# Kernel tuning notes

Hardware: AMD Instinct MI355X
Metric: run time of the kernel (lower is better)

Reference implementation:

```python
import jax, jax.numpy as jnp
import numpy as np

B, S, D, H = 2, 2048, 1024, 16
HD = D // H

def setup_inputs() -> dict:
    key = jax.random.key(0)
    ks = jax.random.split(key, 9)
    s = 1.0 / np.sqrt(D)
    return {
        "x": jax.random.normal(ks[0], (B, S, D), jnp.float32),
        "Wq": jax.random.normal(ks[1], (D, D), jnp.float32) * s,
        "bq": jnp.zeros((D,), jnp.float32),
        "Wk": jax.random.normal(ks[2], (D, D), jnp.float32) * s,
        "bk": jnp.zeros((D,), jnp.float32),
        "Wv": jax.random.normal(ks[3], (D, D), jnp.float32) * s,
        "bv": jnp.zeros((D,), jnp.float32),
        "Wo": jax.random.normal(ks[4], (D, D), jnp.float32) * s,
        "bo": jnp.zeros((D,), jnp.float32),
    }

def reference(x, Wq, bq, Wk, bk, Wv, bv, Wo, bo):
    b, s, d = x.shape
    def split_heads(t):
        return t.reshape(b, s, H, HD).transpose(0, 2, 1, 3)  # [B,H,S,HD]
    q = split_heads(x @ Wq + bq)
    k = split_heads(x @ Wk + bk)
    v = split_heads(x @ Wv + bv)
    scores = jnp.einsum('bhqd,bhkd->bhqk', q, k) / jnp.sqrt(jnp.float32(HD))
    causal = jnp.tril(jnp.ones((s, s), bool))  # True = keep
    scores = jnp.where(causal, scores, -jnp.inf)
    attn = jax.nn.softmax(scores, axis=-1)
    out = jnp.einsum('bhqk,bhkd->bhqd', attn, v)  # [B,H,S,HD]
    out = out.transpose(0, 2, 1, 3).reshape(b, s, d)
    return out @ Wo + bo
```

## Files before the change

kernel.cpp:

```cpp
#include <hip/hip_runtime.h>

typedef unsigned short u16;
typedef unsigned int u32;
typedef __attribute__((ext_vector_type(8))) short bf16x8;
typedef __attribute__((ext_vector_type(4))) float f32x4;
typedef __attribute__((ext_vector_type(16))) float f32x16;

#define BB 2
#define SS 2048
#define DD 1024
#define HH 16
#define HD 64
#define MM (BB * SS)

__device__ inline float u2f(u32 u) { return __uint_as_float(u); }
__device__ inline u16 f2bf(float f) {
  u32 u = __float_as_uint(f);
  return (u16)((u + 0x7fffu + ((u >> 16) & 1u)) >> 16);
}

typedef const __attribute__((address_space(1))) void* gas_ptr;
typedef __attribute__((address_space(3))) void* las_ptr;
__device__ __forceinline__ void gll16(const void* g, void* l) {
  __builtin_amdgcn_global_load_lds((gas_ptr)g, (las_ptr)l, 16, 0, 0);
}

__device__ __forceinline__ u32 pk2(float a, float b) {
  return (__float_as_uint(a) >> 16) | (__float_as_uint(b) & 0xffff0000u);
}

__global__ __launch_bounds__(256) void prep(const float* __restrict__ x, u16* __restrict__ xb,
                                            const float* __restrict__ W0, const float* __restrict__ W1,
                                            const float* __restrict__ W2, const float* __restrict__ W3,
                                            u16* __restrict__ Wt) {
  int z = blockIdx.z;
  int t = threadIdx.x;
  if (z >= 4) {
    int gid = (z - 4) * 256 + blockIdx.y * 16 + blockIdx.x;
    int i = (gid * 256 + t) * 8;
    float4 a = *(const float4*)(x + i);
    float4 b = *(const float4*)(x + i + 4);
    uint4 o;
    o.x = (u32)f2bf(a.x) | ((u32)f2bf(a.y) << 16);
    o.y = (u32)f2bf(a.z) | ((u32)f2bf(a.w) << 16);
    o.z = (u32)f2bf(b.x) | ((u32)f2bf(b.y) << 16);
    o.w = (u32)f2bf(b.z) | ((u32)f2bf(b.w) << 16);
    *(uint4*)(xb + i) = o;
    return;
  }
  const float* W = (z == 0) ? W0 : (z == 1) ? W1 : (z == 2) ? W2 : W3;
  u16* out = Wt + (size_t)z * (DD * DD);
  __shared__ __align__(16) u16 T[64][72];
  int n0 = blockIdx.x * 64, k0 = blockIdx.y * 64;
#pragma unroll
  for (int p = 0; p < 4; ++p) {
    int kr = (t >> 4) + p * 16;
    int c4 = (t & 15) * 4;
    float4 v = *(const float4*)&W[(size_t)(k0 + kr) * DD + n0 + c4];
    T[c4 + 0][kr] = f2bf(v.x);
    T[c4 + 1][kr] = f2bf(v.y);
    T[c4 + 2][kr] = f2bf(v.z);
    T[c4 + 3][kr] = f2bf(v.w);
  }
  __syncthreads();
#pragma unroll
  for (int p = 0; p < 2; ++p) {
    int n = (t >> 3) + p * 32;
    int c8 = (t & 7) * 8;
    uint4 v = *(const uint4*)&T[n][c8];
    *(uint4*)&out[(size_t)(n0 + n) * DD + k0 + c8] = v;
  }
}

__global__ __launch_bounds__(256, 3) void gemm_qkv(const u16* __restrict__ xb, const u16* __restrict__ Wt,
                                                   const float* __restrict__ bq, const float* __restrict__ bk,
                                                   const float* __restrict__ bv,
                                                   u16* __restrict__ Qb, u16* __restrict__ Kb, u16* __restrict__ Vtb) {
  __shared__ __align__(16) u16 As[2][128 * 32];
  __shared__ __align__(16) u16 Bs[2][128 * 32];
  const int tid = threadIdx.x, lane = tid & 63, wv = tid >> 6;
  const int wm = (wv >> 1) * 64, wn = (wv & 1) * 64;
  const int l16 = lane & 15, quad = lane >> 4;

  const int id = blockIdx.x;
  const int xcd = id & 7, inner = id >> 3;
  const int mg = xcd >> 1, ng = xcd & 1;
  const int im = inner & 7, rest = inner >> 3;
  const int in_ = rest & 3, z = rest >> 2;
  const int m0 = (mg * 8 + im) * 128, n0 = (ng * 4 + in_) * 128;

  const u16* Bt = Wt + (size_t)z * (DD * DD);
  const float* bias = (z == 0) ? bq : (z == 1) ? bk : bv;

  const int r0 = tid >> 2, k8 = (tid & 3) << 3;
  const u16* Ap0 = &xb[(size_t)(m0 + r0) * DD + k8];
  const u16* Ap1 = Ap0 + (size_t)64 * DD;
  const u16* Bp0 = &Bt[(size_t)(n0 + r0) * DD + k8];
  const u16* Bp1 = Bp0 + (size_t)64 * DD;

  gll16(Ap0, &As[0][wv * 512]);
  gll16(Ap1, &As[0][2048 + wv * 512]);
  gll16(Bp0, &Bs[0][wv * 512]);
  gll16(Bp1, &Bs[0][2048 + wv * 512]);

  f32x4 acc[4][4];
  f32x4 zero = {0.f, 0.f, 0.f, 0.f};
#pragma unroll
  for (int i = 0; i < 4; ++i)
#pragma unroll
    for (int j = 0; j < 4; ++j) acc[i][j] = zero;

  __syncthreads();

  for (int kk = 0; kk < 32; ++kk) {
    const int cur = kk & 1;
    if (kk + 1 < 32) {
      const int nxt = cur ^ 1;
      const int ko = (kk + 1) * 32;
      gll16(Ap0 + ko, &As[nxt][wv * 512]);
      gll16(Ap1 + ko, &As[nxt][2048 + wv * 512]);
      gll16(Bp0 + ko, &Bs[nxt][wv * 512]);
      gll16(Bp1 + ko, &Bs[nxt][2048 + wv * 512]);
    }
    bf16x8 af[4], bg[4];
#pragma unroll
    for (int i = 0; i < 4; ++i) {
      af[i] = *(const bf16x8*)&As[cur][(wm + i * 16 + l16) * 32 + quad * 8];
      bg[i] = *(const bf16x8*)&Bs[cur][(wn + i * 16 + l16) * 32 + quad * 8];
    }
#pragma unroll
    for (int i = 0; i < 4; ++i)
#pragma unroll
      for (int j = 0; j < 4; ++j)
        acc[i][j] = __builtin_amdgcn_mfma_f32_16x16x32_bf16(af[i], bg[j], acc[i][j], 0, 0, 0);
    __syncthreads();
  }

  const float qsc = (z == 0) ? 0.180336880f : 1.0f;
  if (z == 2) {
#pragma unroll
    for (int i = 0; i < 4; ++i) {
#pragma unroll
      for (int j = 0; j < 4; ++j) {
        int col = n0 + wn + j * 16 + l16;
        float bcol = bias[col];
        int hh = col >> 6, dd = col & 63;
        int row0 = m0 + wm + i * 16;
        int bb = row0 >> 11, s0 = row0 & (SS - 1);
        int sbase = (s0 & ~63) + i * 16 + ((quad & 1) << 3) + ((quad >> 1) << 2);
        size_t base = (((size_t)((bb * HH + hh) * HD + dd)) << 11) + sbase;
        uint2 pv;
        pv.x = (u32)f2bf(acc[i][j][0] + bcol) | ((u32)f2bf(acc[i][j][1] + bcol) << 16);
        pv.y = (u32)f2bf(acc[i][j][2] + bcol) | ((u32)f2bf(acc[i][j][3] + bcol) << 16);
        *(uint2*)&Vtb[base] = pv;
      }
    }
  } else {
    u16* out = (z == 0) ? Qb : Kb;
#pragma unroll
    for (int i = 0; i < 4; ++i) {
#pragma unroll
      for (int j = 0; j < 4; ++j) {
        int col = n0 + wn + j * 16 + l16;
        float bcol = bias[col];
        int hh = col >> 6, dd = col & 63;
#pragma unroll
        for (int r = 0; r < 4; ++r) {
          int row = m0 + wm + i * 16 + quad * 4 + r;
          int bb = row >> 11, s = row & (SS - 1);
          out[((size_t)((bb * HH + hh) * SS + s) << 6) | dd] = f2bf((acc[i][j][r] + bcol) * qsc);
        }
      }
    }
  }
}

__global__ __launch_bounds__(256, 3) void gemm_out(const u16* __restrict__ Ub, const u16* __restrict__ Wot,
                                                   const float* __restrict__ bo, float* __restrict__ out) {
  __shared__ __align__(16) u16 As[2][128 * 32];
  __shared__ __align__(16) u16 Bs[2][64 * 32];
  const int tid = threadIdx.x, lane = tid & 63, wv = tid >> 6;
  const int wm = (wv >> 1) * 64, wn = (wv & 1) * 32;
  const int l16 = lane & 15, quad = lane >> 4;
  const int r0 = tid >> 2, k8 = (tid & 3) << 3;

  const int id = blockIdx.x;
  const int xcd = id & 7, inner = id >> 3;
  const int mg = xcd >> 1, ng = xcd & 1;
  const int im = inner & 7, in_ = inner >> 3;
  const int m0 = (mg * 8 + im) * 128, n0 = (ng * 8 + in_) * 64;

  const u16* Ap0 = &Ub[(size_t)(m0 + r0) * DD + k8];
  const u16* Ap1 = Ap0 + (size_t)64 * DD;
  const u16* Bp0 = &Wot[(size_t)(n0 + r0) * DD + k8];

  gll16(Ap0, &As[0][wv * 512]);
  gll16(Ap1, &As[0][2048 + wv * 512]);
  gll16(Bp0, &Bs[0][wv * 512]);

  f32x4 acc[4][2];
  f32x4 zero = {0.f, 0.f, 0.f, 0.f};
#pragma unroll
  for (int i = 0; i < 4; ++i) { acc[i][0] = zero; acc[i][1] = zero; }

  __syncthreads();

  for (int kk = 0; kk < 32; ++kk) {
    const int cur = kk & 1;
    if (kk + 1 < 32) {
      const int nxt = cur ^ 1;
      const int ko = (kk + 1) * 32;
      gll16(Ap0 + ko, &As[nxt][wv * 512]);
      gll16(Ap1 + ko, &As[nxt][2048 + wv * 512]);
      gll16(Bp0 + ko, &Bs[nxt][wv * 512]);
    }
    bf16x8 af[4], bg[2];
#pragma unroll
    for (int i = 0; i < 4; ++i) af[i] = *(const bf16x8*)&As[cur][(wm + i * 16 + l16) * 32 + quad * 8];
#pragma unroll
    for (int j = 0; j < 2; ++j) bg[j] = *(const bf16x8*)&Bs[cur][(wn + j * 16 + l16) * 32 + quad * 8];
#pragma unroll
    for (int i = 0; i < 4; ++i)
#pragma unroll
      for (int j = 0; j < 2; ++j)
        acc[i][j] = __builtin_amdgcn_mfma_f32_16x16x32_bf16(af[i], bg[j], acc[i][j], 0, 0, 0);
    __syncthreads();
  }

#pragma unroll
  for (int i = 0; i < 4; ++i) {
#pragma unroll
    for (int j = 0; j < 2; ++j) {
      int col = n0 + wn + j * 16 + l16;
      float bcol = bo[col];
#pragma unroll
      for (int r = 0; r < 4; ++r) {
        int row = m0 + wm + i * 16 + quad * 4 + r;
        out[(size_t)row * DD + col] = acc[i][j][r] + bcol;
      }
    }
  }
}

__global__ __launch_bounds__(256, 2) void attention_mfma(const u16* __restrict__ Q, const u16* __restrict__ K,
                                                         const u16* __restrict__ Vt, u16* __restrict__ Uo) {
  const int tid = threadIdx.x, lane = tid & 63, wv = tid >> 6;
  const int l31 = lane & 31, hi = lane >> 5;
  const int bh = blockIdx.x & 31;
  const int b = bh >> 4, h = bh & 15;
  const int g = blockIdx.x >> 5;
  const int qb = (blockIdx.x < 256) ? (15 - g) : (g - 8);
  const int q0 = qb * 128;
  const int qbase = q0 + wv * 32;
  const u16* Qh = Q + (size_t)(b * HH + h) * SS * HD;
  const u16* Kh = K + (size_t)(b * HH + h) * SS * HD;
  const u16* Vh = Vt + (size_t)(b * HH + h) * HD * SS;

  __shared__ __align__(16) u16 K_lds[2][4160];
  __shared__ __align__(16) u16 V_lds[2][4160];
  __shared__ float lsc[128];

  bf16x8 qf[4];
  {
    const u16* qp = &Qh[(size_t)(qbase + l31) * HD + 8 * hi];
#pragma unroll
    for (int m = 0; m < 4; ++m) qf[m] = *(const bf16x8*)(qp + 16 * m);
  }

  f32x16 o0, o1;
#pragma unroll
  for (int i = 0; i < 16; ++i) { o0[i] = 0.f; o1[i] = 0.f; }
  float lsum = 0.f;

  const int sr = tid >> 2, ci = tid & 3;
  const u16* Kg = &Kh[(size_t)sr * HD + ci * 8];
  const u16* Vg = &Vh[(size_t)sr * SS + ci * 8];
  const int ktiles = 2 * qb + 2;
  const int w0 = ci * 520 + sr * 8, w1 = (ci + 4) * 520 + sr * 8;

  uint4 ka = *(const uint4*)Kg, kb = *(const uint4*)(Kg + 32);
  uint4 va = *(const uint4*)Vg, vb = *(const uint4*)(Vg + 32);
  *(uint4*)&K_lds[0][w0] = ka;
  *(uint4*)&K_lds[0][w1] = kb;
  *(uint4*)&V_lds[0][w0] = va;
  *(uint4*)&V_lds[0][w1] = vb;
  {
    const u16* Kn = Kg + (size_t)64 * HD;
    const u16* Vn = Vg + 64;
    ka = *(const uint4*)Kn; kb = *(const uint4*)(Kn + 32);
    va = *(const uint4*)Vn; vb = *(const uint4*)(Vn + 32);
  }
  __syncthreads();

  for (int t = 0; t < ktiles; ++t) {
    const int cur = t & 1;
    if (64 * t <= qbase + 31) {
      f32x16 s0, s1;
#pragma unroll
      for (int i = 0; i < 16; ++i) { s0[i] = 0.f; s1[i] = 0.f; }
#pragma unroll
      for (int m = 0; m < 4; ++m) {
        const u16* kp = &K_lds[cur][(2 * m + hi) * 520 + l31 * 8];
        bf16x8 kf0 = *(const bf16x8*)kp;
        bf16x8 kf1 = *(const bf16x8*)(kp + 256);
        s0 = __builtin_amdgcn_mfma_f32_32x32x16_bf16(kf0, qf[m], s0, 0, 0, 0);
        s1 = __builtin_amdgcn_mfma_f32_32x32x16_bf16(kf1, qf[m], s1, 0, 0, 0);
      }
#pragma unroll
      for (int i = 0; i < 16; ++i) {
        s0[i] = __builtin_amdgcn_exp2f(s0[i]);
        s1[i] = __builtin_amdgcn_exp2f(s1[i]);
      }
      if (64 * t + 63 > qbase) {
        const int qq = qbase + l31, kb0 = 64 * t + 4 * hi;
#pragma unroll
        for (int p = 0; p < 4; ++p)
#pragma unroll
          for (int c = 0; c < 4; ++c) {
            if (kb0 + 8 * p + c > qq) s0[4 * p + c] = 0.f;
            if (kb0 + 32 + 8 * p + c > qq) s1[4 * p + c] = 0.f;
          }
      }
#pragma unroll
      for (int i = 0; i < 16; ++i) lsum += s0[i] + s1[i];

#pragma unroll
      for (int m = 0; m < 4; ++m) {
        const int p0 = 8 * (m & 1);
        union { uint4 u; bf16x8 v; } pa;
        if (m < 2) {
          pa.u.x = pk2(s0[p0 + 0], s0[p0 + 1]);
          pa.u.y = pk2(s0[p0 + 2], s0[p0 + 3]);
          pa.u.z = pk2(s0[p0 + 4], s0[p0 + 5]);
          pa.u.w = pk2(s0[p0 + 6], s0[p0 + 7]);
        } else {
          pa.u.x = pk2(s1[p0 + 0], s1[p0 + 1]);
          pa.u.y = pk2(s1[p0 + 2], s1[p0 + 3]);
          pa.u.z = pk2(s1[p0 + 4], s1[p0 + 5]);
          pa.u.w = pk2(s1[p0 + 6], s1[p0 + 7]);
        }
        const u16* vp = &V_lds[cur][(2 * m + hi) * 520 + l31 * 8];
        bf16x8 vf0 = *(const bf16x8*)vp;
        bf16x8 vf1 = *(const bf16x8*)(vp + 256);
        o0 = __builtin_amdgcn_mfma_f32_32x32x16_bf16(pa.v, vf0, o0, 0, 0, 0);
        o1 = __builtin_amdgcn_mfma_f32_32x32x16_bf16(pa.v, vf1, o1, 0, 0, 0);
      }
    }

    if (t + 1 < ktiles) {
      const int nxt = cur ^ 1;
      *(uint4*)&K_lds[nxt][w0] = ka;
      *(uint4*)&K_lds[nxt][w1] = kb;
      *(uint4*)&V_lds[nxt][w0] = va;
      *(uint4*)&V_lds[nxt][w1] = vb;
      if (t + 2 < ktiles) {
        const u16* Kn = Kg + (size_t)(t + 2) * 64 * HD;
        const u16* Vn = Vg + (t + 2) * 64;
        ka = *(const uint4*)Kn; kb = *(const uint4*)(Kn + 32);
        va = *(const uint4*)Vn; vb = *(const uint4*)(Vn + 32);
      }
    }
    __syncthreads();
  }

  lsum += __shfl_xor(lsum, 32);
  if (hi == 0) lsc[wv * 32 + l31] = 1.0f / lsum;
  __syncthreads();
  f32x4 lv[4];
#pragma unroll
  for (int p = 0; p < 4; ++p) lv[p] = *(const f32x4*)&lsc[wv * 32 + 8 * p + 4 * hi];

  u16* ub = Uo + (size_t)(b * SS) * DD + (h << 6);
#pragma unroll
  for (int p = 0; p < 4; ++p) {
#pragma unroll
    for (int c = 0; c < 4; ++c) {
      int row = qbase + 8 * p + 4 * hi + c;
      ub[(size_t)row * DD + l31] = f2bf(o0[4 * p + c] * lv[p][c]);
      ub[(size_t)row * DD + 32 + l31] = f2bf(o1[4 * p + c] * lv[p][c]);
    }
  }
}

extern "C" void kernel_launch(void* const* d_in, const int* in_sizes, int n_in,
                              void* d_out, int out_size, void* d_ws, size_t ws_size,
                              hipStream_t stream) {
  const float* x  = (const float*)d_in[0];
  const float* Wq = (const float*)d_in[1];
  const float* bq = (const float*)d_in[2];
  const float* Wk = (const float*)d_in[3];
  const float* bk = (const float*)d_in[4];
  const float* Wv = (const float*)d_in[5];
  const float* bv = (const float*)d_in[6];
  const float* Wo = (const float*)d_in[7];
  const float* bo = (const float*)d_in[8];
  float* out = (float*)d_out;

  char* ws = (char*)d_ws;
  u16* xb  = (u16*)(ws);
  u16* Wt  = (u16*)(ws + ((size_t)8 << 20));
  u16* Qb  = (u16*)(ws + ((size_t)16 << 20));
  u16* Kb  = (u16*)(ws + ((size_t)24 << 20));
  u16* Vtb = (u16*)(ws + ((size_t)32 << 20));
  u16* Ub  = (u16*)(ws + ((size_t)40 << 20));

  prep<<<dim3(16, 16, 12), dim3(256), 0, stream>>>(x, xb, Wq, Wk, Wv, Wo, Wt);
  gemm_qkv<<<dim3(768), dim3(256), 0, stream>>>(xb, Wt, bq, bk, bv, Qb, Kb, Vtb);
  attention_mfma<<<dim3(512), dim3(256), 0, stream>>>(Qb, Kb, Vtb, Ub);
  gemm_out<<<dim3(512), dim3(256), 0, stream>>>(Ub, Wt + (size_t)3 * DD * DD, bo, out);
}
```

Baseline: 170.7 us.

## Load K/V fragments straight to registers per wave, dropping LDS staging and barriers

The attention kernel no longer stages K and V tiles through double-buffered shared memory with block-wide barriers. Each wave now loads its own K and V MFMA fragments directly from global memory into registers, prefetching the next tile while computing the current one. It stops at its own causal tile count and raises scheduling priority around the MFMA sections. The softmax normaliser is broadcast with shuffles instead of going through LDS. The four waves of a block now fetch the same K/V from global or L2 separately, so cache traffic and register pressure go up.

```diff
diff --git a/kernel.cpp b/kernel.cpp
--- a/kernel.cpp
+++ b/kernel.cpp
@@ -250,16 +250,11 @@
   const int b = bh >> 4, h = bh & 15;
   const int g = blockIdx.x >> 5;
   const int qb = (blockIdx.x < 256) ? (15 - g) : (g - 8);
-  const int q0 = qb * 128;
-  const int qbase = q0 + wv * 32;
+  const int qbase = qb * 128 + wv * 32;
   const u16* Qh = Q + (size_t)(b * HH + h) * SS * HD;
   const u16* Kh = K + (size_t)(b * HH + h) * SS * HD;
   const u16* Vh = Vt + (size_t)(b * HH + h) * HD * SS;
 
-  __shared__ __align__(16) u16 K_lds[2][4160];
-  __shared__ __align__(16) u16 V_lds[2][4160];
-  __shared__ float lsc[128];
-
   bf16x8 qf[4];
   {
     const u16* qp = &Qh[(size_t)(qbase + l31) * HD + 8 * hi];
@@ -272,103 +267,103 @@
   for (int i = 0; i < 16; ++i) { o0[i] = 0.f; o1[i] = 0.f; }
   float lsum = 0.f;
 
-  const int sr = tid >> 2, ci = tid & 3;
-  const u16* Kg = &Kh[(size_t)sr * HD + ci * 8];
-  const u16* Vg = &Vh[(size_t)sr * SS + ci * 8];
-  const int ktiles = 2 * qb + 2;
-  const int w0 = ci * 520 + sr * 8, w1 = (ci + 4) * 520 + sr * 8;
-
-  uint4 ka = *(const uint4*)Kg, kb = *(const uint4*)(Kg + 32);
-  uint4 va = *(const uint4*)Vg, vb = *(const uint4*)(Vg + 32);
-  *(uint4*)&K_lds[0][w0] = ka;
-  *(uint4*)&K_lds[0][w1] = kb;
-  *(uint4*)&V_lds[0][w0] = va;
-  *(uint4*)&V_lds[0][w1] = vb;
-  {
-    const u16* Kn = Kg + (size_t)64 * HD;
-    const u16* Vn = Vg + 64;
-    ka = *(const uint4*)Kn; kb = *(const uint4*)(Kn + 32);
-    va = *(const uint4*)Vn; vb = *(const uint4*)(Vn + 32);
-  }
-  __syncthreads();
-
-  for (int t = 0; t < ktiles; ++t) {
-    const int cur = t & 1;
-    if (64 * t <= qbase + 31) {
-      f32x16 s0, s1;
-#pragma unroll
-      for (int i = 0; i < 16; ++i) { s0[i] = 0.f; s1[i] = 0.f; }
+  const int ntiles = (qbase + 31) / 64 + 1;
+
+  const u16* Kp = &Kh[(size_t)l31 * HD + 8 * hi];
+  const u16* Vp = &Vh[(size_t)l31 * SS + 8 * hi];
+
+  bf16x8 kc0[4], kc1[4], vc0[4], vc1[4];
+#pragma unroll
+  for (int m = 0; m < 4; ++m) {
+    kc0[m] = *(const bf16x8*)(Kp + 16 * m);
+    kc1[m] = *(const bf16x8*)(Kp + 32 * HD + 16 * m);
+    vc0[m] = *(const bf16x8*)(Vp + 16 * m);
+    vc1[m] = *(const bf16x8*)(Vp + 32 * SS + 16 * m);
+  }
+
+  for (int t = 0; t < ntiles; ++t) {
+    bf16x8 kn0[4], kn1[4], vn0[4], vn1[4];
+    const bool pf = (t + 1 < ntiles);
+    if (pf) {
+      const u16* Kq = Kp + (size_t)(t + 1) * 64 * HD;
+      const u16* Vq = Vp + (t + 1) * 64;
 #pragma unroll
       for (int m = 0; m < 4; ++m) {
-        const u16* kp = &K_lds[cur][(2 * m + hi) * 520 + l31 * 8];
-        bf16x8 kf0 = *(const bf16x8*)kp;
-        bf16x8 kf1 = *(const bf16x8*)(kp + 256);
-        s0 = __builtin_amdgcn_mfma_f32_32x32x16_bf16(kf0, qf[m], s0, 0, 0, 0);
-        s1 = __builtin_amdgcn_mfma_f32_32x32x16_bf16(kf1, qf[m], s1, 0, 0, 0);
-      }
-#pragma unroll
-      for (int i = 0; i < 16; ++i) {
-        s0[i] = __builtin_amdgcn_exp2f(s0[i]);
-        s1[i] = __builtin_amdgcn_exp2f(s1[i]);
-      }
-      if (64 * t + 63 > qbase) {
-        const int qq = qbase + l31, kb0 = 64 * t + 4 * hi;
-#pragma unroll
-        for (int p = 0; p < 4; ++p)
-#pragma unroll
-          for (int c = 0; c < 4; ++c) {
-            if (kb0 + 8 * p + c > qq) s0[4 * p + c] = 0.f;
-            if (kb0 + 32 + 8 * p + c > qq) s1[4 * p + c] = 0.f;
-          }
-      }
-#pragma unroll
-      for (int i = 0; i < 16; ++i) lsum += s0[i] + s1[i];
-
+        kn0[m] = *(const bf16x8*)(Kq + 16 * m);
+        kn1[m] = *(const bf16x8*)(Kq + 32 * HD + 16 * m);
+        vn0[m] = *(const bf16x8*)(Vq + 16 * m);
+        vn1[m] = *(const bf16x8*)(Vq + 32 * SS + 16 * m);
+      }
+    }
+
+    f32x16 s0, s1;
+#pragma unroll
+    for (int i = 0; i < 16; ++i) { s0[i] = 0.f; s1[i] = 0.f; }
+    __builtin_amdgcn_s_setprio(1);
+#pragma unroll
+    for (int m = 0; m < 4; ++m) {
+      s0 = __builtin_amdgcn_mfma_f32_32x32x16_bf16(kc0[m], qf[m], s0, 0, 0, 0);
+      s1 = __builtin_amdgcn_mfma_f32_32x32x16_bf16(kc1[m], qf[m], s1, 0, 0, 0);
+    }
+    __builtin_amdgcn_s_setprio(0);
+
+#pragma unroll
+    for (int i = 0; i < 16; ++i) {
+      s0[i] = __builtin_amdgcn_exp2f(s0[i]);
+      s1[i] = __builtin_amdgcn_exp2f(s1[i]);
+    }
+    if (64 * t + 63 > qbase) {
+      const int qq = qbase + l31, kb0 = 64 * t + 4 * hi;
+#pragma unroll
+      for (int p = 0; p < 4; ++p)
+#pragma unroll
+        for (int c = 0; c < 4; ++c) {
+          if (kb0 + 8 * p + c > qq) s0[4 * p + c] = 0.f;
+          if (kb0 + 32 + 8 * p + c > qq) s1[4 * p + c] = 0.f;
+        }
+    }
+#pragma unroll
+    for (int i = 0; i < 16; ++i) lsum += s0[i] + s1[i];
+
+    __builtin_amdgcn_s_setprio(1);
+#pragma unroll
+    for (int m = 0; m < 4; ++m) {
+      const int p0 = 8 * (m & 1);
+      union { uint4 u; bf16x8 v; } pa;
+      if (m < 2) {
+        pa.u.x = pk2(s0[p0 + 0], s0[p0 + 1]);
+        pa.u.y = pk2(s0[p0 + 2], s0[p0 + 3]);
+        pa.u.z = pk2(s0[p0 + 4], s0[p0 + 5]);
+        pa.u.w = pk2(s0[p0 + 6], s0[p0 + 7]);
+      } else {
+        pa.u.x = pk2(s1[p0 + 0], s1[p0 + 1]);
+        pa.u.y = pk2(s1[p0 + 2], s1[p0 + 3]);
+        pa.u.z = pk2(s1[p0 + 4], s1[p0 + 5]);
+        pa.u.w = pk2(s1[p0 + 6], s1[p0 + 7]);
+      }
+      o0 = __builtin_amdgcn_mfma_f32_32x32x16_bf16(pa.v, vc0[m], o0, 0, 0, 0);
+      o1 = __builtin_amdgcn_mfma_f32_32x32x16_bf16(pa.v, vc1[m], o1, 0, 0, 0);
+    }
+    __builtin_amdgcn_s_setprio(0);
+
+    if (pf) {
 #pragma unroll
       for (int m = 0; m < 4; ++m) {
-        const int p0 = 8 * (m & 1);
-        union { uint4 u; bf16x8 v; } pa;
-        if (m < 2) {
-          pa.u.x = pk2(s0[p0 + 0], s0[p0 + 1]);
-          pa.u.y = pk2(s0[p0 + 2], s0[p0 + 3]);
-          pa.u.z = pk2(s0[p0 + 4], s0[p0 + 5]);
-          pa.u.w = pk2(s0[p0 + 6], s0[p0 + 7]);
-        } else {
-          pa.u.x = pk2(s1[p0 + 0], s1[p0 + 1]);
-          pa.u.y = pk2(s1[p0 + 2], s1[p0 + 3]);
-          pa.u.z = pk2(s1[p0 + 4], s1[p0 + 5]);
-          pa.u.w = pk2(s1[p0 + 6], s1[p0 + 7]);
-        }
-        const u16* vp = &V_lds[cur][(2 * m + hi) * 520 + l31 * 8];
-        bf16x8 vf0 = *(const bf16x8*)vp;
-        bf16x8 vf1 = *(const bf16x8*)(vp + 256);
-        o0 = __builtin_amdgcn_mfma_f32_32x32x16_bf16(pa.v, vf0, o0, 0, 0, 0);
-        o1 = __builtin_amdgcn_mfma_f32_32x32x16_bf16(pa.v, vf1, o1, 0, 0, 0);
-      }
-    }
-
-    if (t + 1 < ktiles) {
-      const int nxt = cur ^ 1;
-      *(uint4*)&K_lds[nxt][w0] = ka;
-      *(uint4*)&K_lds[nxt][w1] = kb;
-      *(uint4*)&V_lds[nxt][w0] = va;
-      *(uint4*)&V_lds[nxt][w1] = vb;
-      if (t + 2 < ktiles) {
-        const u16* Kn = Kg + (size_t)(t + 2) * 64 * HD;
-        const u16* Vn = Vg + (t + 2) * 64;
-        ka = *(const uint4*)Kn; kb = *(const uint4*)(Kn + 32);
-        va = *(const uint4*)Vn; vb = *(const uint4*)(Vn + 32);
-      }
-    }
-    __syncthreads();
+        kc0[m] = kn0[m];
+        kc1[m] = kn1[m];
+        vc0[m] = vn0[m];
+        vc1[m] = vn1[m];
+      }
+    }
   }
 
   lsum += __shfl_xor(lsum, 32);
-  if (hi == 0) lsc[wv * 32 + l31] = 1.0f / lsum;
-  __syncthreads();
-  f32x4 lv[4];
-#pragma unroll
-  for (int p = 0; p < 4; ++p) lv[p] = *(const f32x4*)&lsc[wv * 32 + 8 * p + 4 * hi];
+  const float li = 1.0f / lsum;
+  float linv[4][4];
+#pragma unroll
+  for (int p = 0; p < 4; ++p)
+#pragma unroll
+    for (int c = 0; c < 4; ++c) linv[p][c] = __shfl(li, 8 * p + 4 * hi + c);
 
   u16* ub = Uo + (size_t)(b * SS) * DD + (h << 6);
 #pragma unroll
@@ -376,8 +371,8 @@
 #pragma unroll
     for (int c = 0; c < 4; ++c) {
       int row = qbase + 8 * p + 4 * hi + c;
-      ub[(size_t)row * DD + l31] = f2bf(o0[4 * p + c] * lv[p][c]);
-      ub[(size_t)row * DD + 32 + l31] = f2bf(o1[4 * p + c] * lv[p][c]);
+      ub[(size_t)row * DD + l31] = f2bf(o0[4 * p + c] * linv[p][c]);
+      ub[(size_t)row * DD + 32 + l31] = f2bf(o1[4 * p + c] * linv[p][c]);
     }
   }
 }
```

Measured after the change: 204.2 us. +19.6%, slower.

## Triple-buffer LDS in QKV and output GEMMs with explicit vmcnt waits

Applied to the files above, without the earlier changes.

Both projection GEMMs move from a double-buffered to a three-stage LDS ring, prefetching three K-slices ahead via global_load_lds. Fine-grained s_waitcnt vmcnt counts and raw s_barrier calls replace the full __syncthreads, so two slices of loads can be in flight while MFMAs run. LDS use per block grows by half, which may reduce occupancy under the 3-blocks-per-CU bound. The hand-counted waits assume the compiler issues no other vector memory ops inside the loop.

```diff
diff --git a/kernel.cpp b/kernel.cpp
--- a/kernel.cpp
+++ b/kernel.cpp
@@ -76,8 +76,8 @@
                                                    const float* __restrict__ bq, const float* __restrict__ bk,
                                                    const float* __restrict__ bv,
                                                    u16* __restrict__ Qb, u16* __restrict__ Kb, u16* __restrict__ Vtb) {
-  __shared__ __align__(16) u16 As[2][128 * 32];
-  __shared__ __align__(16) u16 Bs[2][128 * 32];
+  __shared__ __align__(16) u16 As[3 * 4096];
+  __shared__ __align__(16) u16 Bs[3 * 4096];
   const int tid = threadIdx.x, lane = tid & 63, wv = tid >> 6;
   const int wm = (wv >> 1) * 64, wn = (wv & 1) * 64;
   const int l16 = lane & 15, quad = lane >> 4;
@@ -98,10 +98,16 @@
   const u16* Bp0 = &Bt[(size_t)(n0 + r0) * DD + k8];
   const u16* Bp1 = Bp0 + (size_t)64 * DD;
 
-  gll16(Ap0, &As[0][wv * 512]);
-  gll16(Ap1, &As[0][2048 + wv * 512]);
-  gll16(Bp0, &Bs[0][wv * 512]);
-  gll16(Bp1, &Bs[0][2048 + wv * 512]);
+  const int ldst = wv * 512;
+
+#pragma unroll
+  for (int p = 0; p < 3; ++p) {
+    const int ko = p * 32, bo_ = p * 4096;
+    gll16(Ap0 + ko, &As[bo_ + ldst]);
+    gll16(Ap1 + ko, &As[bo_ + 2048 + ldst]);
+    gll16(Bp0 + ko, &Bs[bo_ + ldst]);
+    gll16(Bp1 + ko, &Bs[bo_ + 2048 + ldst]);
+  }
 
   f32x4 acc[4][4];
   f32x4 zero = {0.f, 0.f, 0.f, 0.f};
@@ -110,30 +116,41 @@
 #pragma unroll
     for (int j = 0; j < 4; ++j) acc[i][j] = zero;
 
-  __syncthreads();
-
-  for (int kk = 0; kk < 32; ++kk) {
-    const int cur = kk & 1;
-    if (kk + 1 < 32) {
-      const int nxt = cur ^ 1;
-      const int ko = (kk + 1) * 32;
-      gll16(Ap0 + ko, &As[nxt][wv * 512]);
-      gll16(Ap1 + ko, &As[nxt][2048 + wv * 512]);
-      gll16(Bp0 + ko, &Bs[nxt][wv * 512]);
-      gll16(Bp1 + ko, &Bs[nxt][2048 + wv * 512]);
-    }
+  asm volatile("s_waitcnt vmcnt(8)" ::: "memory");
+  __builtin_amdgcn_s_barrier();
+
+  int cur = 0;
+  for (int t = 0; t < 32; ++t) {
     bf16x8 af[4], bg[4];
+    const int cb = cur * 4096;
 #pragma unroll
     for (int i = 0; i < 4; ++i) {
-      af[i] = *(const bf16x8*)&As[cur][(wm + i * 16 + l16) * 32 + quad * 8];
-      bg[i] = *(const bf16x8*)&Bs[cur][(wn + i * 16 + l16) * 32 + quad * 8];
-    }
+      af[i] = *(const bf16x8*)&As[cb + (wm + i * 16 + l16) * 32 + quad * 8];
+      bg[i] = *(const bf16x8*)&Bs[cb + (wn + i * 16 + l16) * 32 + quad * 8];
+    }
+    asm volatile("s_waitcnt lgkmcnt(0)" ::: "memory");
+    __builtin_amdgcn_s_barrier();
+    if (t + 3 < 32) {
+      const int ko = (t + 3) * 32;
+      gll16(Ap0 + ko, &As[cb + ldst]);
+      gll16(Ap1 + ko, &As[cb + 2048 + ldst]);
+      gll16(Bp0 + ko, &Bs[cb + ldst]);
+      gll16(Bp1 + ko, &Bs[cb + 2048 + ldst]);
+    }
+    __builtin_amdgcn_sched_barrier(0);
 #pragma unroll
     for (int i = 0; i < 4; ++i)
 #pragma unroll
       for (int j = 0; j < 4; ++j)
         acc[i][j] = __builtin_amdgcn_mfma_f32_16x16x32_bf16(af[i], bg[j], acc[i][j], 0, 0, 0);
-    __syncthreads();
+    if (t <= 28)
+      asm volatile("s_waitcnt vmcnt(8)" ::: "memory");
+    else if (t == 29)
+      asm volatile("s_waitcnt vmcnt(4)" ::: "memory");
+    else if (t == 30)
+      asm volatile("s_waitcnt vmcnt(0)" ::: "memory");
+    if (t < 31) __builtin_amdgcn_s_barrier();
+    cur = (cur == 2) ? 0 : cur + 1;
   }
 
   const float qsc = (z == 0) ? 0.180336880f : 1.0f;
@@ -177,8 +194,8 @@
 
 __global__ __launch_bounds__(256, 3) void gemm_out(const u16* __restrict__ Ub, const u16* __restrict__ Wot,
                                                    const float* __restrict__ bo, float* __restrict__ out) {
-  __shared__ __align__(16) u16 As[2][128 * 32];
-  __shared__ __align__(16) u16 Bs[2][64 * 32];
+  __shared__ __align__(16) u16 As[3 * 4096];
+  __shared__ __align__(16) u16 Bs[3 * 2048];
   const int tid = threadIdx.x, lane = tid & 63, wv = tid >> 6;
   const int wm = (wv >> 1) * 64, wn = (wv & 1) * 32;
   const int l16 = lane & 15, quad = lane >> 4;
@@ -194,37 +211,53 @@
   const u16* Ap1 = Ap0 + (size_t)64 * DD;
   const u16* Bp0 = &Wot[(size_t)(n0 + r0) * DD + k8];
 
-  gll16(Ap0, &As[0][wv * 512]);
-  gll16(Ap1, &As[0][2048 + wv * 512]);
-  gll16(Bp0, &Bs[0][wv * 512]);
+  const int ldst = wv * 512;
+
+#pragma unroll
+  for (int p = 0; p < 3; ++p) {
+    const int ko = p * 32;
+    gll16(Ap0 + ko, &As[p * 4096 + ldst]);
+    gll16(Ap1 + ko, &As[p * 4096 + 2048 + ldst]);
+    gll16(Bp0 + ko, &Bs[p * 2048 + ldst]);
+  }
 
   f32x4 acc[4][2];
   f32x4 zero = {0.f, 0.f, 0.f, 0.f};
 #pragma unroll
   for (int i = 0; i < 4; ++i) { acc[i][0] = zero; acc[i][1] = zero; }
 
-  __syncthreads();
-
-  for (int kk = 0; kk < 32; ++kk) {
-    const int cur = kk & 1;
-    if (kk + 1 < 32) {
-      const int nxt = cur ^ 1;
-      const int ko = (kk + 1) * 32;
-      gll16(Ap0 + ko, &As[nxt][wv * 512]);
-      gll16(Ap1 + ko, &As[nxt][2048 + wv * 512]);
-      gll16(Bp0 + ko, &Bs[nxt][wv * 512]);
-    }
+  asm volatile("s_waitcnt vmcnt(6)" ::: "memory");
+  __builtin_amdgcn_s_barrier();
+
+  int cur = 0;
+  for (int t = 0; t < 32; ++t) {
     bf16x8 af[4], bg[2];
 #pragma unroll
-    for (int i = 0; i < 4; ++i) af[i] = *(const bf16x8*)&As[cur][(wm + i * 16 + l16) * 32 + quad * 8];
-#pragma unroll
-    for (int j = 0; j < 2; ++j) bg[j] = *(const bf16x8*)&Bs[cur][(wn + j * 16 + l16) * 32 + quad * 8];
+    for (int i = 0; i < 4; ++i) af[i] = *(const bf16x8*)&As[cur * 4096 + (wm + i * 16 + l16) * 32 + quad * 8];
+#pragma unroll
+    for (int j = 0; j < 2; ++j) bg[j] = *(const bf16x8*)&Bs[cur * 2048 + (wn + j * 16 + l16) * 32 + quad * 8];
+    asm volatile("s_waitcnt lgkmcnt(0)" ::: "memory");
+    __builtin_amdgcn_s_barrier();
+    if (t + 3 < 32) {
+      const int ko = (t + 3) * 32;
+      gll16(Ap0 + ko, &As[cur * 4096 + ldst]);
+      gll16(Ap1 + ko, &As[cur * 4096 + 2048 + ldst]);
+      gll16(Bp0 + ko, &Bs[cur * 2048 + ldst]);
+    }
+    __builtin_amdgcn_sched_barrier(0);
 #pragma unroll
     for (int i = 0; i < 4; ++i)
 #pragma unroll
       for (int j = 0; j < 2; ++j)
         acc[i][j] = __builtin_amdgcn_mfma_f32_16x16x32_bf16(af[i], bg[j], acc[i][j], 0, 0, 0);
-    __syncthreads();
+    if (t <= 28)
+      asm volatile("s_waitcnt vmcnt(6)" ::: "memory");
+    else if (t == 29)
+      asm volatile("s_waitcnt vmcnt(3)" ::: "memory");
+    else if (t == 30)
+      asm volatile("s_waitcnt vmcnt(0)" ::: "memory");
+    if (t < 31) __builtin_amdgcn_s_barrier();
+    cur = (cur == 2) ? 0 : cur + 1;
   }
 
 #pragma unroll
```

Result: no change. 167.8 us, median of 3 (-1.7%).
